# Performance work log

Measured on AMD Instinct MI355X. Metric: run time of the kernel, lower is better.

The kernel has to match this reference:

```python
import jax, jax.numpy as jnp
import numpy as np
from jax.ops import segment_sum, segment_max

N = 100000      # nodes
E = 1600000     # directed edges (before self loops)
H = 4           # attention heads
DIMS = [128, 128, 128, 64]
NEG_SLOPE = 0.2


def setup_inputs() -> dict:
    key = jax.random.key(0)
    ks = jax.random.split(key, 20)
    inp = {}
    inp['x'] = jax.random.normal(ks[0], (N, DIMS[0]), jnp.float32)
    inp['edge_index'] = jax.random.randint(ks[1], (2, E), 0, N, jnp.int32)
    k = 2
    for i in range(3):
        ind, outd = DIMS[i], DIMS[i + 1]
        hd = outd // H
        s = 1.0 / np.sqrt(ind)
        inp[f'W{i}'] = jax.random.uniform(ks[k], (ind, outd), jnp.float32, -s, s); k += 1
        inp[f'a_src{i}'] = jax.random.uniform(ks[k], (H, hd), jnp.float32, -s, s); k += 1
        inp[f'a_dst{i}'] = jax.random.uniform(ks[k], (H, hd), jnp.float32, -s, s); k += 1
        inp[f'b{i}'] = jnp.zeros((outd,), jnp.float32)
    s = 1.0 / np.sqrt(DIMS[-1])
    inp['Wc'] = jax.random.uniform(ks[k], (DIMS[-1], 40), jnp.float32, -s, s)
    inp['bc'] = jnp.zeros((40,), jnp.float32)
    return inp


def _gat_layer(x, W, a_src, a_dst, b, src, dst):
    n = x.shape[0]
    hd = a_src.shape[1]
    h = (x @ W).reshape(n, H, hd)                       # [N,H,hd]
    # per-node attention logits (computed once, gathered per edge)
    al_s = (h * a_src[None]).sum(-1)                    # [N,H]
    al_d = (h * a_dst[None]).sum(-1)                    # [N,H]
    e = jax.nn.leaky_relu(al_s[src] + al_d[dst], NEG_SLOPE)   # [E,H]
    # segment softmax over incoming edges of each destination node
    m = segment_max(e, dst, num_segments=n)             # [N,H]
    ex = jnp.exp(e - m[dst])                            # [E,H]
    denom = segment_sum(ex, dst, num_segments=n)        # [N,H]
    alpha = ex / (denom[dst] + 1e-16)                   # [E,H]
    msg = alpha[:, :, None] * h[src]                    # [E,H,hd]
    out = segment_sum(msg, dst, num_segments=n)         # [N,H,hd]
    return out.reshape(n, H * hd) + b


def reference(x, W0, a_src0, a_dst0, b0, W1, a_src1, a_dst1, b1,
              W2, a_src2, a_dst2, b2, Wc, bc, edge_index):
    n = x.shape[0]
    loops = jnp.arange(n, dtype=edge_index.dtype)       # PyG add_self_loops=True
    src = jnp.concatenate([edge_index[0], loops])
    dst = jnp.concatenate([edge_index[1], loops])
    params = [(W0, a_src0, a_dst0, b0), (W1, a_src1, a_dst1, b1), (W2, a_src2, a_dst2, b2)]
    h = x
    for (W, a_s, a_d, b) in params:
        h = jax.nn.relu(_gat_layer(h, W, a_s, a_d, b, src, dst))
    return h @ Wc + bc
```

## Files before the change

### kernel.cpp

```cpp
#include <hip/hip_runtime.h>
#include <hip/hip_bf16.h>
#include <hip/hip_fp16.h>
#include <stdint.h>

typedef __hip_bfloat16 bf16;
typedef _Float16 f16;
typedef __attribute__((ext_vector_type(8))) _Float16 f16x8;
typedef __attribute__((ext_vector_type(4))) float    f32x4;

__device__ __forceinline__ float us2f(uint16_t u){
  union { uint32_t i; float f; } v; v.i = ((uint32_t)u) << 16; return v.f;
}
__device__ __forceinline__ float bflo(uint32_t u){
  union { uint32_t i; float f; } v; v.i = u << 16; return v.f;
}
__device__ __forceinline__ float bfhi(uint32_t u){
  union { uint32_t i; float f; } v; v.i = u & 0xffff0000u; return v.f;
}
__device__ __forceinline__ uint16_t f2u16(float f){
  union { bf16 b; uint16_t u; } v; v.b = __float2bfloat16(f); return v.u;
}
struct h16 { uint16_t v; };

__device__ __forceinline__ float  ldh (const float* p, size_t i){ return p[i]; }
__device__ __forceinline__ float  ldh (const uint16_t* p, size_t i){ return us2f(p[i]); }
__device__ __forceinline__ float  ldh (const h16* p, size_t i){ return __half2float(((const __half*)p)[i]); }
__device__ __forceinline__ float2 ldh2(const float* p, size_t i){ return ((const float2*)p)[i]; }
__device__ __forceinline__ float2 ldh2(const uint16_t* p, size_t i){
  uint32_t u = ((const uint32_t*)p)[i]; return make_float2(bflo(u), bfhi(u));
}
__device__ __forceinline__ float2 ldh2(const h16* p, size_t i){
  __half2 u = ((const __half2*)p)[i];
  return make_float2(__low2float(u), __high2float(u));
}
__device__ __forceinline__ void sth (float* p, size_t i, float v){ p[i] = v; }
__device__ __forceinline__ void sth (uint16_t* p, size_t i, float v){ p[i] = f2u16(v); }
__device__ __forceinline__ void sth (h16* p, size_t i, float v){ ((__half*)p)[i] = __float2half(v); }
__device__ __forceinline__ void sth2(float* p, size_t i, float2 v){ ((float2*)p)[i] = v; }
__device__ __forceinline__ void sth2(uint16_t* p, size_t i, float2 v){
  ((uint32_t*)p)[i] = (uint32_t)f2u16(v.x) | ((uint32_t)f2u16(v.y) << 16);
}
__device__ __forceinline__ void sth2(h16* p, size_t i, float2 v){
  ((__half2*)p)[i] = __float22half2_rn(v);
}
__device__ __forceinline__ void ld4(const float* p, size_t i4, float* o){
  float4 v = ((const float4*)p)[i4]; o[0]=v.x; o[1]=v.y; o[2]=v.z; o[3]=v.w;
}
__device__ __forceinline__ void ld4(const uint16_t* p, size_t i4, float* o){
  uint2 u = ((const uint2*)p)[i4];
  o[0]=bflo(u.x); o[1]=bfhi(u.x); o[2]=bflo(u.y); o[3]=bfhi(u.y);
}
__device__ __forceinline__ void ld4(const h16* p, size_t i4, float* o){
  __half2 u0 = ((const __half2*)p)[i4*2];
  __half2 u1 = ((const __half2*)p)[i4*2+1];
  o[0]=__low2float(u0); o[1]=__high2float(u0);
  o[2]=__low2float(u1); o[3]=__high2float(u1);
}
__device__ __forceinline__ void ld2v(const float* p, size_t i2, float* o){
  float2 v = ((const float2*)p)[i2]; o[0]=v.x; o[1]=v.y;
}
__device__ __forceinline__ void ld2v(const uint16_t* p, size_t i2, float* o){
  uint32_t u = ((const uint32_t*)p)[i2]; o[0]=bflo(u); o[1]=bfhi(u);
}
__device__ __forceinline__ void ld2v(const h16* p, size_t i2, float* o){
  __half2 u = ((const __half2*)p)[i2]; o[0]=__low2float(u); o[1]=__high2float(u);
}
__device__ __forceinline__ void st4(float* p, size_t i4, const float* o){
  ((float4*)p)[i4] = make_float4(o[0],o[1],o[2],o[3]);
}
__device__ __forceinline__ void st4(uint16_t* p, size_t i4, const float* o){
  uint2 u;
  u.x = (uint32_t)f2u16(o[0]) | ((uint32_t)f2u16(o[1]) << 16);
  u.y = (uint32_t)f2u16(o[2]) | ((uint32_t)f2u16(o[3]) << 16);
  ((uint2*)p)[i4] = u;
}
__device__ __forceinline__ void st4(h16* p, size_t i4, const float* o){
  ((__half2*)p)[i4*2]   = __float22half2_rn(make_float2(o[0],o[1]));
  ((__half2*)p)[i4*2+1] = __float22half2_rn(make_float2(o[2],o[3]));
}
__device__ __forceinline__ void ld8(const float* p, size_t i, float* o){
  float4 a = ((const float4*)(p+i))[0];
  float4 b = ((const float4*)(p+i))[1];
  o[0]=a.x; o[1]=a.y; o[2]=a.z; o[3]=a.w; o[4]=b.x; o[5]=b.y; o[6]=b.z; o[7]=b.w;
}
__device__ __forceinline__ void ld8(const uint16_t* p, size_t i, float* o){
  uint4 u = *(const uint4*)(p+i);
  o[0]=bflo(u.x); o[1]=bfhi(u.x); o[2]=bflo(u.y); o[3]=bfhi(u.y);
  o[4]=bflo(u.z); o[5]=bfhi(u.z); o[6]=bflo(u.w); o[7]=bfhi(u.w);
}
__device__ __forceinline__ void ld8(const h16* p, size_t i, float* o){
  const __half2* q = (const __half2*)(p+i);
  #pragma unroll
  for (int j=0;j<4;j++){ __half2 u=q[j]; o[2*j]=__low2float(u); o[2*j+1]=__high2float(u); }
}

__global__ void detect_kernel(const uint32_t* __restrict__ x, int* __restrict__ flag){
  int lane = threadIdx.x;
  uint32_t w = x[lane];
  uint32_t e = (w >> 7) & 0xffu;
  bool looks_bf16 = (e >= 118 && e <= 134);
  unsigned long long m = __ballot(looks_bf16);
  if (lane == 0) flag[0] = (__popcll(m) >= 32) ? 0 : 1;
}

__global__ void edetect_kernel(const uint32_t* __restrict__ ei, int* __restrict__ eflag){
  int lane = threadIdx.x;
  uint32_t w = ei[lane];
  bool ok = (lane & 1) ? (w == 0u) : true;
  unsigned long long m = __ballot(ok);
  if (lane == 0) eflag[0] = (__popcll(m) == 64) ? 1 : 0;
}

struct PP {
  const void* src[14];
  int off[14];
  int cnt[14];
};

__global__ void cvt_params_kernel(PP pp, float* __restrict__ dst, const int* __restrict__ flag){
  int b = blockIdx.x;
  int cnt = pp.cnt[b];
  float* d = dst + pp.off[b];
  if (flag[0] != 0){
    const float* s = (const float*)pp.src[b];
    for (int i = threadIdx.x; i < cnt; i += 256) d[i] = s[i];
  } else {
    const uint16_t* s = (const uint16_t*)pp.src[b];
    for (int i = threadIdx.x; i < cnt; i += 256) d[i] = us2f(s[i]);
  }
}

__global__ void wfrag_kernel(const float* __restrict__ W, uint16_t* __restrict__ wh,
                             uint16_t* __restrict__ wl, int K, int M){
  int e = blockIdx.x * 256 + threadIdx.x;
  int CT = M >> 4, KC = K >> 5;
  if (e >= KC*CT*64) return;
  int l = e & 63, t = e >> 6;
  int ct = t % CT, c = t / CT;
  int kbase = c*32 + (l>>4)*8;
  int m = ct*16 + (l&15);
  #pragma unroll
  for (int i=0;i<8;i++){
    float w = W[(size_t)(kbase+i)*M + m];
    f16 h = (f16)w;
    f16 r = (f16)(w - (float)h);
    union { f16 f; uint16_t u; } ch, cr; ch.f = h; cr.f = r;
    wh[(size_t)e*8 + i] = ch.u;
    wl[(size_t)e*8 + i] = cr.u;
  }
}

__global__ void count_kernel(const int* __restrict__ ei, const int* __restrict__ eflag,
                             int* __restrict__ counts, int* __restrict__ rank,
                             int E, int n){
  int i = blockIdx.x * 256 + threadIdx.x;
  if (i >= E + n) return;
  int d;
  if (i < E) d = eflag[0] ? ei[2*(size_t)E + 2*(size_t)i] : ei[(size_t)E + i];
  else       d = i - E;
  rank[i] = atomicAdd(&counts[d], 1);
}

#define SCAN_BS 256
#define SCAN_CHUNK 1024

__global__ void scan1_kernel(const int* __restrict__ counts, int* __restrict__ offs,
                             int* __restrict__ bsums, int n){
  __shared__ int sdata[SCAN_BS];
  int b = blockIdx.x, t = threadIdx.x;
  int base = b * SCAN_CHUNK + t * 4;
  int v[4]; int s = 0;
  #pragma unroll
  for (int j=0;j<4;j++){ int idx = base+j; v[j] = (idx<n)? counts[idx] : 0; s += v[j]; }
  sdata[t] = s;
  __syncthreads();
  for (int off=1; off<SCAN_BS; off<<=1){
    int x = (t>=off)? sdata[t-off] : 0;
    __syncthreads();
    sdata[t] += x;
    __syncthreads();
  }
  int run = sdata[t] - s;
  #pragma unroll
  for (int j=0;j<4;j++){ int idx = base+j; if (idx<n) offs[idx] = run; run += v[j]; }
  if (t == SCAN_BS-1) bsums[b] = sdata[t];
}

__global__ void scan2_kernel(int* __restrict__ bsums, int nb){
  __shared__ int sdata[1024];
  int t = threadIdx.x;
  int v = (t<nb)? bsums[t] : 0;
  sdata[t] = v;
  __syncthreads();
  for (int off=1; off<1024; off<<=1){
    int x = (t>=off)? sdata[t-off] : 0;
    __syncthreads();
    sdata[t] += x;
    __syncthreads();
  }
  if (t<nb) bsums[t] = sdata[t] - v;
}

__global__ void scan3_kernel(int* __restrict__ offs, const int* __restrict__ bsums,
                             int n, int total){
  int i = blockIdx.x * 256 + threadIdx.x;
  if (i < n) offs[i] += bsums[i / SCAN_CHUNK];
  if (i == n) offs[n] = total;
}

__global__ void fill_kernel(const int* __restrict__ ei, const int* __restrict__ eflag,
                            const int* __restrict__ offs, const int* __restrict__ rank,
                            int* __restrict__ csr, int E, int n){
  int i = blockIdx.x * 256 + threadIdx.x;
  if (i >= E + n) return;
  int s, d;
  if (i < E){
    if (eflag[0]){ s = ei[2*(size_t)i]; d = ei[2*(size_t)E + 2*(size_t)i]; }
    else         { s = ei[i];           d = ei[(size_t)E + i]; }
  } else { s = i - E; d = i - E; }
  csr[offs[d] + rank[i]] = s;
}

template<int K, int M, bool DET, typename TA, typename TC>
__global__ __launch_bounds__(256) void gemm_mfma(const void* __restrict__ Ap,
    const uint16_t* __restrict__ whb, const uint16_t* __restrict__ wlb,
    TC* __restrict__ C, int n, const int* __restrict__ flag){
  constexpr int CT = M/16;
  constexpr int KC = K/32;
  constexpr int RT = 2;
  int tid = threadIdx.x;
  int wv  = tid >> 6, l = tid & 63;
  int lr  = l & 15, kg = l >> 4;
  int r0  = blockIdx.x*(64*RT) + wv*(16*RT);

  bool f32 = DET ? (flag[0] != 0) : false;
  const uint16_t* Au = (const uint16_t*)Ap;
  const float*    Af = (const float*)Ap;
  const TA*       At = (const TA*)Ap;
  const f16x8* Wh = (const f16x8*)whb;
  const f16x8* Wl = (const f16x8*)wlb;

  f32x4 acc[RT][CT];
  #pragma unroll
  for (int rt=0;rt<RT;rt++)
    #pragma unroll
    for (int ct=0;ct<CT;ct++) acc[rt][ct] = (f32x4){0.f,0.f,0.f,0.f};

  for (int c=0; c<KC; c++){
    f16x8 ah[RT], al[RT];
    #pragma unroll
    for (int rt=0;rt<RT;rt++){
      int arow = r0 + rt*16 + lr;
      if (arow > n-1) arow = n-1;
      size_t idx = (size_t)arow*K + c*32 + kg*8;
      float av[8];
      if (DET){
        if (f32) ld8(Af, idx, av);
        else     ld8(Au, idx, av);
      } else {
        ld8(At, idx, av);
      }
      #pragma unroll
      for (int i=0;i<8;i++){
        f16 h = (f16)av[i];
        ah[rt][i] = h;
        al[rt][i] = (f16)(av[i] - (float)h);
      }
    }
    #pragma unroll
    for (int ct=0;ct<CT;ct++){
      f16x8 bh = Wh[(size_t)(c*CT + ct)*64 + l];
      f16x8 bl = Wl[(size_t)(c*CT + ct)*64 + l];
      #pragma unroll
      for (int rt=0;rt<RT;rt++){
        acc[rt][ct] = __builtin_amdgcn_mfma_f32_16x16x32_f16(ah[rt], bh, acc[rt][ct], 0, 0, 0);
        acc[rt][ct] = __builtin_amdgcn_mfma_f32_16x16x32_f16(al[rt], bh, acc[rt][ct], 0, 0, 0);
        acc[rt][ct] = __builtin_amdgcn_mfma_f32_16x16x32_f16(ah[rt], bl, acc[rt][ct], 0, 0, 0);
      }
    }
  }

  #pragma unroll
  for (int rt=0;rt<RT;rt++){
    #pragma unroll
    for (int r=0;r<4;r++){
      int orow = r0 + rt*16 + kg*4 + r;
      if (orow < n){
        #pragma unroll
        for (int ct=0;ct<CT;ct++)
          sth(C, (size_t)orow*M + ct*16 + lr, acc[rt][ct][r]);
      }
    }
  }
}

template<int OUTD, int HD, typename T>
__global__ void logits_kernel(const T* __restrict__ hW, const float* __restrict__ a_src,
                              const float* __restrict__ a_dst, float* __restrict__ als,
                              float* __restrict__ ald, int n){
  int i = blockIdx.x * 256 + threadIdx.x;
  if (i >= n*4) return;
  int node = i >> 2, h = i & 3;
  const T* hp = hW + (size_t)node*OUTD + h*HD;
  float ss = 0.f, sd = 0.f;
  #pragma unroll
  for (int d2=0; d2<HD/2; d2++){
    float2 v = ldh2(hp, d2);
    int b = h*HD + 2*d2;
    ss += v.x*a_src[b] + v.y*a_src[b+1];
    sd += v.x*a_dst[b] + v.y*a_dst[b+1];
  }
  als[i] = ss; ald[i] = sd;
}

template<int OUTD, typename TIN, typename TOUT>
__global__ __launch_bounds__(256) void aggregate_kernel(const TIN* __restrict__ hW,
            const float* __restrict__ als, const float* __restrict__ ald,
            const int* __restrict__ offs, const int* __restrict__ csr,
            const float* __restrict__ bias, TOUT* __restrict__ hout, int n){
  constexpr int VEC = OUTD / 32;
  int wid = (blockIdx.x * 256 + threadIdx.x) >> 6;
  if (wid >= n) return;
  int lane = threadIdx.x & 63;
  int half = lane >> 5;
  int l2   = lane & 31;
  int h    = l2 >> 3;
  int beg = offs[wid], end = offs[wid+1];
  float adh = ald[(size_t)wid*4 + h];

  float acc[VEC];
  #pragma unroll
  for (int k=0;k<VEC;k++) acc[k] = 0.f;
  float den = 0.f;

  int last = end - 1;
  for (int j = beg + half; j < end; j += 8){
    int j1 = j+2, j2 = j+4, j3 = j+6;
    bool p1 = j1 < end, p2 = j2 < end, p3 = j3 < end;
    int s0 = csr[j];
    int s1 = csr[p1 ? j1 : last];
    int s2 = csr[p2 ? j2 : last];
    int s3 = csr[p3 ? j3 : last];
    float v0[VEC], v1[VEC], v2[VEC], v3[VEC];
    if constexpr (VEC == 4){
      ld4(hW, (size_t)s0*32 + l2, v0);
      ld4(hW, (size_t)s1*32 + l2, v1);
      ld4(hW, (size_t)s2*32 + l2, v2);
      ld4(hW, (size_t)s3*32 + l2, v3);
    } else {
      ld2v(hW, (size_t)s0*32 + l2, v0);
      ld2v(hW, (size_t)s1*32 + l2, v1);
      ld2v(hW, (size_t)s2*32 + l2, v2);
      ld2v(hW, (size_t)s3*32 + l2, v3);
    }
    float e0 = als[(size_t)s0*4 + h] + adh;
    float e1 = als[(size_t)s1*4 + h] + adh;
    float e2 = als[(size_t)s2*4 + h] + adh;
    float e3 = als[(size_t)s3*4 + h] + adh;
    e0 = (e0>0.f)? e0 : 0.2f*e0;
    e1 = (e1>0.f)? e1 : 0.2f*e1;
    e2 = (e2>0.f)? e2 : 0.2f*e2;
    e3 = (e3>0.f)? e3 : 0.2f*e3;
    float ex0 = __expf(e0);
    float ex1 = p1 ? __expf(e1) : 0.f;
    float ex2 = p2 ? __expf(e2) : 0.f;
    float ex3 = p3 ? __expf(e3) : 0.f;
    den += (ex0 + ex1) + (ex2 + ex3);
    #pragma unroll
    for (int k=0;k<VEC;k++){
      acc[k] = fmaf(ex0, v0[k], acc[k]);
      acc[k] = fmaf(ex1, v1[k], acc[k]);
      acc[k] = fmaf(ex2, v2[k], acc[k]);
      acc[k] = fmaf(ex3, v3[k], acc[k]);
    }
  }

  den += __shfl_xor(den, 32);
  #pragma unroll
  for (int k=0;k<VEC;k++) acc[k] += __shfl_xor(acc[k], 32);

  if (half == 0){
    float inv = 1.f / (den + 1e-16f);
    float o[VEC];
    if constexpr (VEC == 4){
      const float4 bv = ((const float4*)bias)[l2];
      o[0] = fmaf(acc[0], inv, bv.x);
      o[1] = fmaf(acc[1], inv, bv.y);
      o[2] = fmaf(acc[2], inv, bv.z);
      o[3] = fmaf(acc[3], inv, bv.w);
      #pragma unroll
      for (int k=0;k<4;k++) o[k] = (o[k]>0.f)? o[k] : 0.f;
      st4(hout, (size_t)wid*32 + l2, o);
    } else {
      const float2 bv = ((const float2*)bias)[l2];
      o[0] = fmaf(acc[0], inv, bv.x);
      o[1] = fmaf(acc[1], inv, bv.y);
      o[0] = (o[0]>0.f)? o[0] : 0.f;
      o[1] = (o[1]>0.f)? o[1] : 0.f;
      sth2(hout, (size_t)wid*32 + l2, make_float2(o[0], o[1]));
    }
  }
}

template<typename T>
__global__ __launch_bounds__(256) void classifier_kernel(const T* __restrict__ h,
      const float* __restrict__ Wc, const float* __restrict__ bc,
      float* __restrict__ out, int n){
  __shared__ float As[128*65];
  __shared__ float Ws[64*40];
  __shared__ float bs[40];
  int t = threadIdx.x;
  int r0b = blockIdx.x * 128;

  for (int i=t; i<2560; i+=256) Ws[i] = Wc[i];
  if (t < 40) bs[t] = bc[t];

  for (int i=t; i < 128*64; i += 256){
    int r = i >> 6, k = i & 63;
    int gr = r0b + r;
    float a = 0.f;
    if (gr < n) a = ldh(h, (size_t)gr*64 + k);
    As[r*65 + k] = a;
  }
  __syncthreads();

  int tx = t & 7;
  int ty = t >> 3;
  float acc[4][5];
  #pragma unroll
  for (int r=0;r<4;r++)
    #pragma unroll
    for (int c=0;c<5;c++) acc[r][c] = 0.f;

  #pragma unroll 8
  for (int k=0; k<64; k++){
    float a0 = As[(ty*4+0)*65 + k];
    float a1 = As[(ty*4+1)*65 + k];
    float a2 = As[(ty*4+2)*65 + k];
    float a3 = As[(ty*4+3)*65 + k];
    float w[5];
    #pragma unroll
    for (int c=0;c<5;c++) w[c] = Ws[k*40 + tx*5 + c];
    #pragma unroll
    for (int c=0;c<5;c++){
      acc[0][c] = fmaf(a0, w[c], acc[0][c]);
      acc[1][c] = fmaf(a1, w[c], acc[1][c]);
      acc[2][c] = fmaf(a2, w[c], acc[2][c]);
      acc[3][c] = fmaf(a3, w[c], acc[3][c]);
    }
  }

  #pragma unroll
  for (int r=0;r<4;r++){
    int gr = r0b + ty*4 + r;
    if (gr < n){
      #pragma unroll
      for (int c=0;c<5;c++)
        out[(size_t)gr*40 + tx*5 + c] = acc[r][c] + bs[tx*5 + c];
    }
  }
}

template<typename TM, typename TO>
static void run_pipeline(void* const* d_in, int ei_idx, int pbase, int n, int E,
                         void* d_out, int out_size, void* d_ws, size_t ws_size,
                         hipStream_t stream){
  const void* x = d_in[0];
  const int* ei = (const int*)d_in[ei_idx];
  float* out = (float*)d_out;
  int Etot = E + n;

  char* p = (char*)d_ws;
  auto alloc = [&](size_t bytes)->char* {
    char* r = p; p += (bytes + 255) & ~(size_t)255; return r;
  };
  int*   flag   = (int*)  alloc(256);
  int*   eflag  = (int*)  alloc(256);
  int*   counts = (int*)  alloc((size_t)n * 4);
  float* als    = (float*)alloc((size_t)n * 16);
  float* ald    = (float*)alloc((size_t)n * 16);
  float* prm    = (float*)alloc(48000 * 4);
  uint16_t* wh0 = (uint16_t*)alloc(16384 * 2);
  uint16_t* wl0 = (uint16_t*)alloc(16384 * 2);
  uint16_t* wh1 = (uint16_t*)alloc(16384 * 2);
  uint16_t* wl1 = (uint16_t*)alloc(16384 * 2);
  uint16_t* wh2 = (uint16_t*)alloc(8192 * 2);
  uint16_t* wl2 = (uint16_t*)alloc(8192 * 2);

  size_t csr_b  = ((size_t)Etot * 4 + 255) & ~(size_t)255;
  size_t offs_b = ((size_t)(n + 1) * 4 + 255) & ~(size_t)255;
  size_t rank_b = ((size_t)Etot * 4 + 255) & ~(size_t)255;
  size_t out_bytes = (size_t)out_size * 4;
  int *csr, *offs, *rank, *bsums;
  if (csr_b + offs_b + rank_b + 4096 <= out_bytes){
    char* q = (char*)d_out;
    csr   = (int*)q;
    offs  = (int*)(q + csr_b);
    rank  = (int*)(q + csr_b + offs_b);
    bsums = (int*)(q + csr_b + offs_b + rank_b);
  } else {
    csr   = (int*)alloc((size_t)Etot * 4);
    offs  = (int*)alloc((size_t)(n + 1) * 4);
    rank  = (int*)alloc((size_t)Etot * 4);
    bsums = (int*)alloc(4096);
  }
  TM* bufMid = (TM*)alloc((size_t)n * 128 * sizeof(TM));
  TO* bufOut = (TO*)alloc((size_t)n * 128 * sizeof(TO));

  PP pp;
  static const int cnts[14] = {16384,128,128,128, 16384,128,128,128, 8192,64,64,64, 2560,40};
  int off = 0;
  for (int i = 0; i < 14; i++){
    pp.src[i] = d_in[pbase + i];
    pp.cnt[i] = cnts[i];
    pp.off[i] = off;
    off += cnts[i];
  }
  const float* W0  = prm + pp.off[0];
  const float* as0 = prm + pp.off[1];
  const float* ad0 = prm + pp.off[2];
  const float* b0  = prm + pp.off[3];
  const float* W1  = prm + pp.off[4];
  const float* as1 = prm + pp.off[5];
  const float* ad1 = prm + pp.off[6];
  const float* b1  = prm + pp.off[7];
  const float* W2  = prm + pp.off[8];
  const float* as2 = prm + pp.off[9];
  const float* ad2 = prm + pp.off[10];
  const float* b2  = prm + pp.off[11];
  const float* Wc  = prm + pp.off[12];
  const float* bc  = prm + pp.off[13];

  hipMemsetAsync(counts, 0, (size_t)n * 4, stream);

  detect_kernel<<<1, 64, 0, stream>>>((const uint32_t*)x, flag);
  edetect_kernel<<<1, 64, 0, stream>>>((const uint32_t*)ei, eflag);
  cvt_params_kernel<<<14, 256, 0, stream>>>(pp, prm, flag);
  wfrag_kernel<<<8, 256, 0, stream>>>(W0, wh0, wl0, 128, 128);
  wfrag_kernel<<<8, 256, 0, stream>>>(W1, wh1, wl1, 128, 128);
  wfrag_kernel<<<4, 256, 0, stream>>>(W2, wh2, wl2, 128, 64);

  count_kernel<<<(Etot + 255)/256, 256, 0, stream>>>(ei, eflag, counts, rank, E, n);
  int nb = (n + SCAN_CHUNK - 1) / SCAN_CHUNK;
  scan1_kernel<<<nb, SCAN_BS, 0, stream>>>(counts, offs, bsums, n);
  scan2_kernel<<<1, 1024, 0, stream>>>(bsums, nb);
  scan3_kernel<<<(n + 1 + 255)/256, 256, 0, stream>>>(offs, bsums, n, Etot);
  fill_kernel<<<(Etot + 255)/256, 256, 0, stream>>>(ei, eflag, offs, rank, csr, E, n);

  int gg   = (n + 127) / 128;
  int log_grid = (n*4 + 255) / 256;
  int agg_grid = (n + 3) / 4;
  int cls_grid = (n + 127) / 128;

  gemm_mfma<128,128,true,TO,TM><<<gg, 256, 0, stream>>>(x, wh0, wl0, bufMid, n, flag);
  logits_kernel<128,32,TM><<<log_grid, 256, 0, stream>>>(bufMid, as0, ad0, als, ald, n);
  aggregate_kernel<128,TM,TO><<<agg_grid, 256, 0, stream>>>(bufMid, als, ald, offs, csr, b0, bufOut, n);

  gemm_mfma<128,128,false,TO,TM><<<gg, 256, 0, stream>>>(bufOut, wh1, wl1, bufMid, n, flag);
  logits_kernel<128,32,TM><<<log_grid, 256, 0, stream>>>(bufMid, as1, ad1, als, ald, n);
  aggregate_kernel<128,TM,TO><<<agg_grid, 256, 0, stream>>>(bufMid, als, ald, offs, csr, b1, bufOut, n);

  gemm_mfma<128,64,false,TO,TM><<<gg, 256, 0, stream>>>(bufOut, wh2, wl2, bufMid, n, flag);
  logits_kernel<64,16,TM><<<log_grid, 256, 0, stream>>>(bufMid, as2, ad2, als, ald, n);
  aggregate_kernel<64,TM,TO><<<agg_grid, 256, 0, stream>>>(bufMid, als, ald, offs, csr, b2, bufOut, n);

  classifier_kernel<TO><<<cls_grid, 256, 0, stream>>>(bufOut, Wc, bc, out, n);
}

extern "C" void kernel_launch(void* const* d_in, const int* in_sizes, int n_in,
                              void* d_out, int out_size, void* d_ws, size_t ws_size,
                              hipStream_t stream) {
  int n = in_sizes[0] / 128;

  int ei_idx, pbase;
  if (n_in >= 2 && in_sizes[1] > 1000000) { ei_idx = 1;        pbase = 2; }
  else                                    { ei_idx = n_in - 1; pbase = 1; }
  int E = in_sizes[ei_idx] / 2;

  size_t base = 512
              + (((size_t)n*4  + 255) & ~(size_t)255)
              + 2*(((size_t)n*16 + 255) & ~(size_t)255)
              + ((48000*4 + 255) & ~(size_t)255)
              + 4*((16384*2 + 255) & ~(size_t)255)
              + 2*((8192*2 + 255) & ~(size_t)255)
              + 65536
              + 3*(((size_t)(E + n)*4 + 255) & ~(size_t)255);
  size_t f32buf  = ((size_t)n*128*4 + 255) & ~(size_t)255;
  size_t h16buf  = ((size_t)n*128*2 + 255) & ~(size_t)255;

  if (ws_size >= base + f32buf + h16buf)
    run_pipeline<h16, float>(d_in, ei_idx, pbase, n, E, d_out, out_size, d_ws, ws_size, stream);
  else
    run_pipeline<h16, uint16_t>(d_in, ei_idx, pbase, n, E, d_out, out_size, d_ws, ws_size, stream);
}
```

Before: 586.1 us.

## Use MFMA for classifier, merge detect/wfrag launches, keep fp16 gathers packed

```diff
diff --git a/kernel.cpp b/kernel.cpp
--- a/kernel.cpp
+++ b/kernel.cpp
@@ -6,6 +6,8 @@
 typedef __hip_bfloat16 bf16;
 typedef _Float16 f16;
 typedef __attribute__((ext_vector_type(8))) _Float16 f16x8;
+typedef __attribute__((ext_vector_type(4))) _Float16 f16x4;
+typedef __attribute__((ext_vector_type(2))) _Float16 f16x2;
 typedef __attribute__((ext_vector_type(4))) float    f32x4;
 
 __device__ __forceinline__ float us2f(uint16_t u){
@@ -43,6 +45,9 @@
 __device__ __forceinline__ void sth2(h16* p, size_t i, float2 v){
   ((__half2*)p)[i] = __float22half2_rn(v);
 }
+template<typename T> struct vtt { using t = float; };
+template<> struct vtt<h16> { using t = f16; };
+
 __device__ __forceinline__ void ld4(const float* p, size_t i4, float* o){
   float4 v = ((const float4*)p)[i4]; o[0]=v.x; o[1]=v.y; o[2]=v.z; o[3]=v.w;
 }
@@ -50,11 +55,9 @@
   uint2 u = ((const uint2*)p)[i4];
   o[0]=bflo(u.x); o[1]=bfhi(u.x); o[2]=bflo(u.y); o[3]=bfhi(u.y);
 }
-__device__ __forceinline__ void ld4(const h16* p, size_t i4, float* o){
-  __half2 u0 = ((const __half2*)p)[i4*2];
-  __half2 u1 = ((const __half2*)p)[i4*2+1];
-  o[0]=__low2float(u0); o[1]=__high2float(u0);
-  o[2]=__low2float(u1); o[3]=__high2float(u1);
+__device__ __forceinline__ void ld4(const h16* p, size_t i4, f16* o){
+  f16x4 v = ((const f16x4*)p)[i4];
+  o[0]=v[0]; o[1]=v[1]; o[2]=v[2]; o[3]=v[3];
 }
 __device__ __forceinline__ void ld2v(const float* p, size_t i2, float* o){
   float2 v = ((const float2*)p)[i2]; o[0]=v.x; o[1]=v.y;
@@ -62,8 +65,8 @@
 __device__ __forceinline__ void ld2v(const uint16_t* p, size_t i2, float* o){
   uint32_t u = ((const uint32_t*)p)[i2]; o[0]=bflo(u); o[1]=bfhi(u);
 }
-__device__ __forceinline__ void ld2v(const h16* p, size_t i2, float* o){
-  __half2 u = ((const __half2*)p)[i2]; o[0]=__low2float(u); o[1]=__high2float(u);
+__device__ __forceinline__ void ld2v(const h16* p, size_t i2, f16* o){
+  f16x2 v = ((const f16x2*)p)[i2]; o[0]=v[0]; o[1]=v[1];
 }
 __device__ __forceinline__ void st4(float* p, size_t i4, const float* o){
   ((float4*)p)[i4] = make_float4(o[0],o[1],o[2],o[3]);
@@ -94,21 +97,22 @@
   for (int j=0;j<4;j++){ __half2 u=q[j]; o[2*j]=__low2float(u); o[2*j+1]=__high2float(u); }
 }
 
-__global__ void detect_kernel(const uint32_t* __restrict__ x, int* __restrict__ flag){
-  int lane = threadIdx.x;
-  uint32_t w = x[lane];
-  uint32_t e = (w >> 7) & 0xffu;
-  bool looks_bf16 = (e >= 118 && e <= 134);
-  unsigned long long m = __ballot(looks_bf16);
-  if (lane == 0) flag[0] = (__popcll(m) >= 32) ? 0 : 1;
-}
-
-__global__ void edetect_kernel(const uint32_t* __restrict__ ei, int* __restrict__ eflag){
-  int lane = threadIdx.x;
-  uint32_t w = ei[lane];
-  bool ok = (lane & 1) ? (w == 0u) : true;
-  unsigned long long m = __ballot(ok);
-  if (lane == 0) eflag[0] = (__popcll(m) == 64) ? 1 : 0;
+__global__ void detect2_kernel(const uint32_t* __restrict__ x, const uint32_t* __restrict__ ei,
+                               int* __restrict__ flag, int* __restrict__ eflag){
+  int t = threadIdx.x;
+  if (t < 64){
+    uint32_t w = x[t];
+    uint32_t e = (w >> 7) & 0xffu;
+    bool looks_bf16 = (e >= 118 && e <= 134);
+    unsigned long long m = __ballot(looks_bf16);
+    if (t == 0) flag[0] = (__popcll(m) >= 32) ? 0 : 1;
+  } else {
+    int lane = t - 64;
+    uint32_t w = ei[lane];
+    bool ok = (lane & 1) ? (w == 0u) : true;
+    unsigned long long m = __ballot(ok);
+    if (lane == 0) eflag[0] = (__popcll(m) == 64) ? 1 : 0;
+  }
 }
 
 struct PP {
@@ -130,20 +134,34 @@
   }
 }
 
-__global__ void wfrag_kernel(const float* __restrict__ W, uint16_t* __restrict__ wh,
-                             uint16_t* __restrict__ wl, int K, int M){
-  int e = blockIdx.x * 256 + threadIdx.x;
-  int CT = M >> 4, KC = K >> 5;
+struct WF {
+  int src[4];
+  int dst[4];
+  int cnt[4];
+  int K[4], Ms[4], Mp[4];
+  int blk0[5];
+};
+
+__global__ void wfrag4_kernel(const float* __restrict__ prm, uint16_t* __restrict__ whl, WF wf){
+  int b = blockIdx.x;
+  int w = 3;
+  if (b < wf.blk0[1]) w = 0; else if (b < wf.blk0[2]) w = 1; else if (b < wf.blk0[3]) w = 2;
+  int e = (b - wf.blk0[w])*256 + threadIdx.x;
+  int CT = wf.Mp[w] >> 4, KC = wf.K[w] >> 5;
   if (e >= KC*CT*64) return;
+  const float* W = prm + wf.src[w];
+  uint16_t* wh = whl + wf.dst[w];
+  uint16_t* wl = wh + wf.cnt[w];
+  int Ms = wf.Ms[w];
   int l = e & 63, t = e >> 6;
   int ct = t % CT, c = t / CT;
   int kbase = c*32 + (l>>4)*8;
   int m = ct*16 + (l&15);
   #pragma unroll
   for (int i=0;i<8;i++){
-    float w = W[(size_t)(kbase+i)*M + m];
-    f16 h = (f16)w;
-    f16 r = (f16)(w - (float)h);
+    float v = (m < Ms) ? W[(size_t)(kbase+i)*Ms + m] : 0.f;
+    f16 h = (f16)v;
+    f16 r = (f16)(v - (float)h);
     union { f16 f; uint16_t u; } ch, cr; ch.f = h; cr.f = r;
     wh[(size_t)e*8 + i] = ch.u;
     wl[(size_t)e*8 + i] = cr.u;
@@ -294,6 +312,70 @@
   }
 }
 
+template<typename TA>
+__global__ __launch_bounds__(256) void gemm_cls(const TA* __restrict__ A,
+    const uint16_t* __restrict__ whb, const uint16_t* __restrict__ wlb,
+    const float* __restrict__ bc, float* __restrict__ out, int n){
+  constexpr int CT = 3, KC = 2, RT = 2;
+  int tid = threadIdx.x;
+  int wv  = tid >> 6, l = tid & 63;
+  int lr  = l & 15, kg = l >> 4;
+  int r0  = blockIdx.x*128 + wv*32;
+  const f16x8* Wh = (const f16x8*)whb;
+  const f16x8* Wl = (const f16x8*)wlb;
+
+  f32x4 acc[RT][CT];
+  #pragma unroll
+  for (int rt=0;rt<RT;rt++)
+    #pragma unroll
+    for (int ct=0;ct<CT;ct++) acc[rt][ct] = (f32x4){0.f,0.f,0.f,0.f};
+
+  for (int c=0; c<KC; c++){
+    f16x8 ah[RT], al[RT];
+    #pragma unroll
+    for (int rt=0;rt<RT;rt++){
+      int arow = r0 + rt*16 + lr;
+      if (arow > n-1) arow = n-1;
+      size_t idx = (size_t)arow*64 + c*32 + kg*8;
+      float av[8];
+      ld8(A, idx, av);
+      #pragma unroll
+      for (int i=0;i<8;i++){
+        f16 h = (f16)av[i];
+        ah[rt][i] = h;
+        al[rt][i] = (f16)(av[i] - (float)h);
+      }
+    }
+    #pragma unroll
+    for (int ct=0;ct<CT;ct++){
+      f16x8 bh = Wh[(size_t)(c*CT + ct)*64 + l];
+      f16x8 bl = Wl[(size_t)(c*CT + ct)*64 + l];
+      #pragma unroll
+      for (int rt=0;rt<RT;rt++){
+        acc[rt][ct] = __builtin_amdgcn_mfma_f32_16x16x32_f16(ah[rt], bh, acc[rt][ct], 0, 0, 0);
+        acc[rt][ct] = __builtin_amdgcn_mfma_f32_16x16x32_f16(al[rt], bh, acc[rt][ct], 0, 0, 0);
+        acc[rt][ct] = __builtin_amdgcn_mfma_f32_16x16x32_f16(ah[rt], bl, acc[rt][ct], 0, 0, 0);
+      }
+    }
+  }
+
+  #pragma unroll
+  for (int rt=0;rt<RT;rt++){
+    #pragma unroll
+    for (int r=0;r<4;r++){
+      int orow = r0 + rt*16 + kg*4 + r;
+      if (orow < n){
+        #pragma unroll
+        for (int ct=0;ct<CT;ct++){
+          int col = ct*16 + lr;
+          if (col < 40)
+            out[(size_t)orow*40 + col] = acc[rt][ct][r] + bc[col];
+        }
+      }
+    }
+  }
+}
+
 template<int OUTD, int HD, typename T>
 __global__ void logits_kernel(const T* __restrict__ hW, const float* __restrict__ a_src,
                               const float* __restrict__ a_dst, float* __restrict__ als,
@@ -319,6 +401,7 @@
             const int* __restrict__ offs, const int* __restrict__ csr,
             const float* __restrict__ bias, TOUT* __restrict__ hout, int n){
   constexpr int VEC = OUTD / 32;
+  using VT = typename vtt<TIN>::t;
   int wid = (blockIdx.x * 256 + threadIdx.x) >> 6;
   if (wid >= n) return;
   int lane = threadIdx.x & 63;
@@ -341,7 +424,7 @@
     int s1 = csr[p1 ? j1 : last];
     int s2 = csr[p2 ? j2 : last];
     int s3 = csr[p3 ? j3 : last];
-    float v0[VEC], v1[VEC], v2[VEC], v3[VEC];
+    VT v0[VEC], v1[VEC], v2[VEC], v3[VEC];
     if constexpr (VEC == 4){
       ld4(hW, (size_t)s0*32 + l2, v0);
       ld4(hW, (size_t)s1*32 + l2, v1);
@@ -368,10 +451,10 @@
     den += (ex0 + ex1) + (ex2 + ex3);
     #pragma unroll
     for (int k=0;k<VEC;k++){
-      acc[k] = fmaf(ex0, v0[k], acc[k]);
-      acc[k] = fmaf(ex1, v1[k], acc[k]);
-      acc[k] = fmaf(ex2, v2[k], acc[k]);
-      acc[k] = fmaf(ex3, v3[k], acc[k]);
+      acc[k] = fmaf(ex0, (float)v0[k], acc[k]);
+      acc[k] = fmaf(ex1, (float)v1[k], acc[k]);
+      acc[k] = fmaf(ex2, (float)v2[k], acc[k]);
+      acc[k] = fmaf(ex3, (float)v3[k], acc[k]);
     }
   }
 
@@ -402,65 +485,6 @@
   }
 }
 
-template<typename T>
-__global__ __launch_bounds__(256) void classifier_kernel(const T* __restrict__ h,
-      const float* __restrict__ Wc, const float* __restrict__ bc,
-      float* __restrict__ out, int n){
-  __shared__ float As[128*65];
-  __shared__ float Ws[64*40];
-  __shared__ float bs[40];
-  int t = threadIdx.x;
-  int r0b = blockIdx.x * 128;
-
-  for (int i=t; i<2560; i+=256) Ws[i] = Wc[i];
-  if (t < 40) bs[t] = bc[t];
-
-  for (int i=t; i < 128*64; i += 256){
-    int r = i >> 6, k = i & 63;
-    int gr = r0b + r;
-    float a = 0.f;
-    if (gr < n) a = ldh(h, (size_t)gr*64 + k);
-    As[r*65 + k] = a;
-  }
-  __syncthreads();
-
-  int tx = t & 7;
-  int ty = t >> 3;
-  float acc[4][5];
-  #pragma unroll
-  for (int r=0;r<4;r++)
-    #pragma unroll
-    for (int c=0;c<5;c++) acc[r][c] = 0.f;
-
-  #pragma unroll 8
-  for (int k=0; k<64; k++){
-    float a0 = As[(ty*4+0)*65 + k];
-    float a1 = As[(ty*4+1)*65 + k];
-    float a2 = As[(ty*4+2)*65 + k];
-    float a3 = As[(ty*4+3)*65 + k];
-    float w[5];
-    #pragma unroll
-    for (int c=0;c<5;c++) w[c] = Ws[k*40 + tx*5 + c];
-    #pragma unroll
-    for (int c=0;c<5;c++){
-      acc[0][c] = fmaf(a0, w[c], acc[0][c]);
-      acc[1][c] = fmaf(a1, w[c], acc[1][c]);
-      acc[2][c] = fmaf(a2, w[c], acc[2][c]);
-      acc[3][c] = fmaf(a3, w[c], acc[3][c]);
-    }
-  }
-
-  #pragma unroll
-  for (int r=0;r<4;r++){
-    int gr = r0b + ty*4 + r;
-    if (gr < n){
-      #pragma unroll
-      for (int c=0;c<5;c++)
-        out[(size_t)gr*40 + tx*5 + c] = acc[r][c] + bs[tx*5 + c];
-    }
-  }
-}
-
 template<typename TM, typename TO>
 static void run_pipeline(void* const* d_in, int ei_idx, int pbase, int n, int E,
                          void* d_out, int out_size, void* d_ws, size_t ws_size,
@@ -480,12 +504,7 @@
   float* als    = (float*)alloc((size_t)n * 16);
   float* ald    = (float*)alloc((size_t)n * 16);
   float* prm    = (float*)alloc(48000 * 4);
-  uint16_t* wh0 = (uint16_t*)alloc(16384 * 2);
-  uint16_t* wl0 = (uint16_t*)alloc(16384 * 2);
-  uint16_t* wh1 = (uint16_t*)alloc(16384 * 2);
-  uint16_t* wl1 = (uint16_t*)alloc(16384 * 2);
-  uint16_t* wh2 = (uint16_t*)alloc(8192 * 2);
-  uint16_t* wl2 = (uint16_t*)alloc(8192 * 2);
+  uint16_t* whl = (uint16_t*)alloc(88064 * 2);
 
   size_t csr_b  = ((size_t)Etot * 4 + 255) & ~(size_t)255;
   size_t offs_b = ((size_t)(n + 1) * 4 + 255) & ~(size_t)255;
@@ -520,25 +539,37 @@
   const float* as0 = prm + pp.off[1];
   const float* ad0 = prm + pp.off[2];
   const float* b0  = prm + pp.off[3];
-  const float* W1  = prm + pp.off[4];
   const float* as1 = prm + pp.off[5];
   const float* ad1 = prm + pp.off[6];
   const float* b1  = prm + pp.off[7];
-  const float* W2  = prm + pp.off[8];
   const float* as2 = prm + pp.off[9];
   const float* ad2 = prm + pp.off[10];
   const float* b2  = prm + pp.off[11];
-  const float* Wc  = prm + pp.off[12];
   const float* bc  = prm + pp.off[13];
 
+  uint16_t* wh0 = whl;
+  uint16_t* wl0 = whl + 16384;
+  uint16_t* wh1 = whl + 32768;
+  uint16_t* wl1 = whl + 49152;
+  uint16_t* wh2 = whl + 65536;
+  uint16_t* wl2 = whl + 73728;
+  uint16_t* whc = whl + 81920;
+  uint16_t* wlc = whl + 84992;
+
   hipMemsetAsync(counts, 0, (size_t)n * 4, stream);
 
-  detect_kernel<<<1, 64, 0, stream>>>((const uint32_t*)x, flag);
-  edetect_kernel<<<1, 64, 0, stream>>>((const uint32_t*)ei, eflag);
+  detect2_kernel<<<1, 128, 0, stream>>>((const uint32_t*)x, (const uint32_t*)ei, flag, eflag);
   cvt_params_kernel<<<14, 256, 0, stream>>>(pp, prm, flag);
-  wfrag_kernel<<<8, 256, 0, stream>>>(W0, wh0, wl0, 128, 128);
-  wfrag_kernel<<<8, 256, 0, stream>>>(W1, wh1, wl1, 128, 128);
-  wfrag_kernel<<<4, 256, 0, stream>>>(W2, wh2, wl2, 128, 64);
+
+  WF wf;
+  wf.src[0]=pp.off[0]; wf.src[1]=pp.off[4]; wf.src[2]=pp.off[8]; wf.src[3]=pp.off[12];
+  wf.dst[0]=0; wf.dst[1]=32768; wf.dst[2]=65536; wf.dst[3]=81920;
+  wf.cnt[0]=16384; wf.cnt[1]=16384; wf.cnt[2]=8192; wf.cnt[3]=3072;
+  wf.K[0]=128; wf.K[1]=128; wf.K[2]=128; wf.K[3]=64;
+  wf.Ms[0]=128; wf.Ms[1]=128; wf.Ms[2]=64; wf.Ms[3]=40;
+  wf.Mp[0]=128; wf.Mp[1]=128; wf.Mp[2]=64; wf.Mp[3]=48;
+  wf.blk0[0]=0; wf.blk0[1]=8; wf.blk0[2]=16; wf.blk0[3]=20; wf.blk0[4]=22;
+  wfrag4_kernel<<<22, 256, 0, stream>>>(prm, whl, wf);
 
   count_kernel<<<(Etot + 255)/256, 256, 0, stream>>>(ei, eflag, counts, rank, E, n);
   int nb = (n + SCAN_CHUNK - 1) / SCAN_CHUNK;
@@ -550,7 +581,6 @@
   int gg   = (n + 127) / 128;
   int log_grid = (n*4 + 255) / 256;
   int agg_grid = (n + 3) / 4;
-  int cls_grid = (n + 127) / 128;
 
   gemm_mfma<128,128,true,TO,TM><<<gg, 256, 0, stream>>>(x, wh0, wl0, bufMid, n, flag);
   logits_kernel<128,32,TM><<<log_grid, 256, 0, stream>>>(bufMid, as0, ad0, als, ald, n);
@@ -564,7 +594,7 @@
   logits_kernel<64,16,TM><<<log_grid, 256, 0, stream>>>(bufMid, as2, ad2, als, ald, n);
   aggregate_kernel<64,TM,TO><<<agg_grid, 256, 0, stream>>>(bufMid, als, ald, offs, csr, b2, bufOut, n);
 
-  classifier_kernel<TO><<<cls_grid, 256, 0, stream>>>(bufOut, Wc, bc, out, n);
+  gemm_cls<TO><<<gg, 256, 0, stream>>>(bufOut, whc, wlc, bc, out, n);
 }
 
 extern "C" void kernel_launch(void* const* d_in, const int* in_sizes, int n_in,
@@ -581,8 +611,7 @@
               + (((size_t)n*4  + 255) & ~(size_t)255)
               + 2*(((size_t)n*16 + 255) & ~(size_t)255)
               + ((48000*4 + 255) & ~(size_t)255)
-              + 4*((16384*2 + 255) & ~(size_t)255)
-              + 2*((8192*2 + 255) & ~(size_t)255)
+              + ((88064*2 + 255) & ~(size_t)255)
               + 65536
               + 3*(((size_t)(E + n)*4 + 255) & ~(size_t)255);
   size_t f32buf  = ((size_t)n*128*4 + 255) & ~(size_t)255;
```

Result: faster. 555.9 us (-5.2%).
